# Optimization experiments

Hardware: AMD Instinct MI355X
Metric: run time of the kernel (lower is better)

Reference implementation:

```python
import jax, jax.numpy as jnp
import numpy as np

N = 50000
E = 800000


def gcn_layer(x, W, b, row, col):
    # Linear transform first (as in CustomGCNLayer.forward)
    h = x @ W + b  # [N, out]
    # Segment-mean over incoming edges grouped by destination node `col`;
    # out[i] = mean(h[row[col == i]]) if node i has in-edges else h[i].
    s = jax.ops.segment_sum(h[row], col, num_segments=N)              # [N, out]
    cnt = jax.ops.segment_sum(jnp.ones((row.shape[0],), h.dtype), col, num_segments=N)  # [N]
    mean = s / jnp.maximum(cnt, 1.0)[:, None]
    return jnp.where(cnt[:, None] > 0, mean, h)


def setup_inputs() -> dict:
    key = jax.random.key(0)
    ks = jax.random.split(key, 6)
    x = jax.random.normal(ks[0], (N, 128), dtype=jnp.float32)
    edge_index = jax.random.randint(ks[1], (2, E), 0, N, dtype=jnp.int64)
    # Glorot-ish scaled weights
    W1 = jax.random.normal(ks[2], (128, 128), dtype=jnp.float32) * (1.0 / np.sqrt(128))
    b1 = jnp.zeros((128,), jnp.float32)
    W2 = jax.random.normal(ks[3], (128, 128), dtype=jnp.float32) * (1.0 / np.sqrt(128))
    b2 = jnp.zeros((128,), jnp.float32)
    W3 = jax.random.normal(ks[4], (128, 64), dtype=jnp.float32) * (1.0 / np.sqrt(128))
    b3 = jnp.zeros((64,), jnp.float32)
    return {"x": x, "edge_index": edge_index, "W1": W1, "b1": b1,
            "W2": W2, "b2": b2, "W3": W3, "b3": b3}


def reference(x, edge_index, W1, b1, W2, b2, W3, b3):
    row, col = edge_index[0], edge_index[1]
    h = jax.nn.relu(gcn_layer(x, W1, b1, row, col))
    # Dropout layers run in eval mode for the reference (identity).
    h = jax.nn.relu(gcn_layer(h, W2, b2, row, col))
    h = gcn_layer(h, W3, b3, row, col)
    return jax.nn.log_softmax(h, axis=1)
```

## Files before the change

### kernel.cpp

```cpp
#include <hip/hip_runtime.h>
#include <hip/hip_bf16.h>


typedef __attribute__((ext_vector_type(8))) short short8v;
typedef __attribute__((ext_vector_type(4))) float f32x4;

#define NPART 256

static __device__ __forceinline__ ushort f2bf(float f) {
    __hip_bfloat16 h = __float2bfloat16(f);
    return *reinterpret_cast<ushort*>(&h);
}
static __device__ __forceinline__ float bf_lo(uint u) { return __uint_as_float(u << 16); }
static __device__ __forceinline__ float bf_hi(uint u) { return __uint_as_float(u & 0xffff0000u); }

static __device__ __forceinline__ void gemm1_body(
    const float* __restrict__ X, const float* __restrict__ W,
    const float* __restrict__ bias, ushort* __restrict__ Y, int n,
    int wid, int lane) {
    int r0 = wid * 16;
    if (r0 >= n) return;
    int arow = r0 + (lane & 15);
    if (arow >= n) arow = n - 1;
    int kb = lane >> 4;
    int c  = lane & 15;

    f32x4 acc[8];
#pragma unroll
    for (int ct = 0; ct < 8; ++ct) acc[ct] = (f32x4)(0.f);

#pragma unroll
    for (int kt = 0; kt < 4; ++kt) {
        const float* ap = &X[(size_t)arow * 128 + kt * 32 + kb * 8];
        float4 a0 = *(const float4*)ap;
        float4 a1 = *(const float4*)(ap + 4);
        union { short8v v; ushort u[8]; } av;
        av.u[0] = f2bf(a0.x); av.u[1] = f2bf(a0.y);
        av.u[2] = f2bf(a0.z); av.u[3] = f2bf(a0.w);
        av.u[4] = f2bf(a1.x); av.u[5] = f2bf(a1.y);
        av.u[6] = f2bf(a1.z); av.u[7] = f2bf(a1.w);
#pragma unroll
        for (int ct = 0; ct < 8; ++ct) {
            union { short8v v; ushort u[8]; } bv;
#pragma unroll
            for (int j = 0; j < 8; ++j)
                bv.u[j] = f2bf(W[(size_t)(kt * 32 + kb * 8 + j) * 128 + ct * 16 + c]);
            acc[ct] = __builtin_amdgcn_mfma_f32_16x16x32_bf16(av.v, bv.v, acc[ct], 0, 0, 0);
        }
    }

    int rg = lane >> 4;
#pragma unroll
    for (int ct = 0; ct < 8; ++ct) {
        float bvs = bias[ct * 16 + c];
#pragma unroll
        for (int j = 0; j < 4; ++j) {
            int r = r0 + rg * 4 + j;
            if (r < n) Y[(size_t)r * 128 + ct * 16 + c] = f2bf(acc[ct][j] + bvs);
        }
    }
}

__global__ __launch_bounds__(256) void fused_pa(
    const int* __restrict__ col, int* __restrict__ Gmat,
    const float* __restrict__ x, const float* __restrict__ W1,
    const float* __restrict__ b1, ushort* __restrict__ hbuf,
    const float* __restrict__ W2, ushort* __restrict__ Wf2,
    const float* __restrict__ W3, ushort* __restrict__ Wf3,
    int n, int E, int NBKT, int ECH, int GB) {
    __shared__ uint hist[1024];
    int b = blockIdx.x, t = threadIdx.x;
    if (b < NPART) {
        for (int i = t; i < NBKT; i += 256) hist[i] = 0;
        __syncthreads();
        int e0 = b * ECH, e1 = min(e0 + ECH, E);
        for (int e = e0 + t; e < e1; e += 256)
            atomicAdd(&hist[col[e] >> 6], 1u);
        __syncthreads();
        for (int i = t; i < NBKT; i += 256)
            Gmat[i * NPART + b] = (int)hist[i];
        return;
    }
    b -= NPART;
    if (b < GB) {
        int wid = (b * 256 + t) >> 6;
        gemm1_body(x, W1, b1, hbuf, n, wid, t & 63);
        return;
    }
    b -= GB;
    const float* W; ushort* Wf; int OUT; int tid;
    if (b < 8) { W = W2; Wf = Wf2; OUT = 128; tid = b * 256 + t; }
    else       { W = W3; Wf = Wf3; OUT = 64;  tid = (b - 8) * 256 + t; }
    int CT = OUT >> 4;
    int total = 4 * CT * 64;
    if (tid >= total) return;
    int kt   = tid / (CT * 64);
    int rem  = tid % (CT * 64);
    int ct   = rem >> 6;
    int lane = rem & 63;
    int c  = lane & 15;
    int kb = lane >> 4;
    ushort tmp[8];
#pragma unroll
    for (int j = 0; j < 8; ++j)
        tmp[j] = f2bf(W[(kt * 32 + kb * 8 + j) * OUT + ct * 16 + c]);
    uint4 o;
    o.x = ((uint)tmp[1] << 16) | tmp[0];
    o.y = ((uint)tmp[3] << 16) | tmp[2];
    o.z = ((uint)tmp[5] << 16) | tmp[4];
    o.w = ((uint)tmp[7] << 16) | tmp[6];
    ((uint4*)Wf)[tid] = o;
}

__global__ void scanA_partial(const int* __restrict__ g, int* __restrict__ bsum, int M) {
    __shared__ int lds[256];
    int i = blockIdx.x * 256 + threadIdx.x;
    int v = (i < M) ? g[i] : 0;
    lds[threadIdx.x] = v;
    __syncthreads();
    for (int s = 128; s > 0; s >>= 1) {
        if (threadIdx.x < s) lds[threadIdx.x] += lds[threadIdx.x + s];
        __syncthreads();
    }
    if (threadIdx.x == 0) bsum[blockIdx.x] = lds[0];
}

__global__ void scan_bsums_big(int* __restrict__ bsum, int nb) {
    __shared__ int ts[256];
    int t = threadIdx.x;
    int v[4]; int s = 0;
#pragma unroll
    for (int j = 0; j < 4; ++j) {
        int i = t * 4 + j;
        v[j] = (i < nb) ? bsum[i] : 0;
        s += v[j];
    }
    ts[t] = s;
    __syncthreads();
    for (int off = 1; off < 256; off <<= 1) {
        int u = (t >= off) ? ts[t - off] : 0;
        __syncthreads();
        ts[t] += u;
        __syncthreads();
    }
    int run = ts[t] - s;
#pragma unroll
    for (int j = 0; j < 4; ++j) {
        int i = t * 4 + j;
        if (i < nb) { int old = v[j]; bsum[i] = run; run += old; }
    }
}

__global__ void scanA_final(int* __restrict__ g, const int* __restrict__ bsum, int M) {
    __shared__ int lds[256];
    int t = threadIdx.x;
    int i = blockIdx.x * 256 + t;
    int v = (i < M) ? g[i] : 0;
    lds[t] = v;
    __syncthreads();
    for (int off = 1; off < 256; off <<= 1) {
        int u = (t >= off) ? lds[t - off] : 0;
        __syncthreads();
        lds[t] += u;
        __syncthreads();
    }
    if (i < M) g[i] = lds[t] - v + bsum[blockIdx.x];
}

__global__ __launch_bounds__(256) void pa2_scatter(
    const int* __restrict__ row, const int* __restrict__ col,
    const int* __restrict__ Gscan, uint* __restrict__ coarse,
    int E, int NBKT, int ECH) {
    __shared__ uint cur[1024];
    int p = blockIdx.x, t = threadIdx.x;
    for (int i = t; i < NBKT; i += 256) cur[i] = (uint)Gscan[i * NPART + p];
    __syncthreads();
    int e0 = p * ECH, e1 = min(e0 + ECH, E);
    for (int e = e0 + t; e < e1; e += 256) {
        int d = col[e];
        uint slot = atomicAdd(&cur[d >> 6], 1u);
        coarse[slot] = ((uint)(d & 63) << 16) | (uint)(row[e] & 0xFFFF);
    }
}

__global__ __launch_bounds__(256) void pb_fine(
    const uint* __restrict__ coarse, const int* __restrict__ Gscan,
    int* __restrict__ cnt, int* __restrict__ start,
    ushort* __restrict__ srclist16, int n, int E, int NBKT) {
    __shared__ uint c64[64];
    int b = blockIdx.x, t = threadIdx.x;
    int lo = Gscan[b * NPART];
    int hi = (b + 1 < NBKT) ? Gscan[(b + 1) * NPART] : E;
    if (t < 64) c64[t] = 0;
    __syncthreads();
    for (int i = lo + t; i < hi; i += 256)
        atomicAdd(&c64[coarse[i] >> 16], 1u);
    __syncthreads();
    if (t < 64) {
        uint v = c64[t];
        uint x = v;
#pragma unroll
        for (int off = 1; off < 64; off <<= 1) {
            uint u = __shfl_up(x, off);
            if (t >= off) x += u;
        }
        uint excl = x - v;
        int node = b * 64 + t;
        if (node < n) { cnt[node] = (int)v; start[node] = lo + (int)excl; }
        c64[t] = excl;
    }
    __syncthreads();
    for (int i = lo + t; i < hi; i += 256) {
        uint u  = coarse[i];
        uint dl = u >> 16;
        uint slot = atomicAdd(&c64[dl], 1u);
        srclist16[lo + slot] = (ushort)u;
    }
}

template <int OUT>
__global__ __launch_bounds__(256) void gemm_mfma(
    const ushort* __restrict__ X, const ushort* __restrict__ Wf,
    const float* __restrict__ bias, ushort* __restrict__ Y, int n) {
    constexpr int CT = OUT / 16;
    int wid  = (blockIdx.x * 256 + threadIdx.x) >> 6;
    int lane = threadIdx.x & 63;
    int r0 = wid * 16;
    if (r0 >= n) return;
    int arow = r0 + (lane & 15);
    if (arow >= n) arow = n - 1;
    int kb = lane >> 4;

    f32x4 acc[CT];
#pragma unroll
    for (int ct = 0; ct < CT; ++ct) acc[ct] = (f32x4)(0.f);

#pragma unroll
    for (int kt = 0; kt < 4; ++kt) {
        short8v a = *(const short8v*)&X[(size_t)arow * 128 + kt * 32 + kb * 8];
#pragma unroll
        for (int ct = 0; ct < CT; ++ct) {
            short8v b = *(const short8v*)&Wf[(size_t)((kt * CT + ct) * 64 + lane) * 8];
            acc[ct] = __builtin_amdgcn_mfma_f32_16x16x32_bf16(a, b, acc[ct], 0, 0, 0);
        }
    }

    int c  = lane & 15;
    int rg = lane >> 4;
#pragma unroll
    for (int ct = 0; ct < CT; ++ct) {
        float bv = bias[ct * 16 + c];
#pragma unroll
        for (int j = 0; j < 4; ++j) {
            int r = r0 + rg * 4 + j;
            if (r < n) Y[(size_t)r * OUT + ct * 16 + c] = f2bf(acc[ct][j] + bv);
        }
    }
}

template <bool RELU>
__global__ __launch_bounds__(256) void agg128_bf16(
    const ushort* __restrict__ h, const int* __restrict__ start,
    const int* __restrict__ cnt, const ushort* __restrict__ srclist16,
    ushort* __restrict__ out, int n) {
    int wid  = (blockIdx.x * blockDim.x + threadIdx.x) >> 6;
    int lane = threadIdx.x & 63;
    if (wid >= n) return;
    const uint* h32 = (const uint*)h;
    int s0 = start[wid];
    int c  = cnt[wid];
    float ax = 0.f, ay = 0.f;
    for (int base = 0; base < c; base += 64) {
        int m = c - base;
        if (m > 64) m = 64;
        int idx = (int)srclist16[s0 + base + (lane < m ? lane : 0)];
        int e = 0;
        for (; e + 8 <= m; e += 8) {
            int i0 = __shfl(idx, e + 0), i1 = __shfl(idx, e + 1);
            int i2 = __shfl(idx, e + 2), i3 = __shfl(idx, e + 3);
            int i4 = __shfl(idx, e + 4), i5 = __shfl(idx, e + 5);
            int i6 = __shfl(idx, e + 6), i7 = __shfl(idx, e + 7);
            uint u0 = h32[(size_t)i0 * 64 + lane];
            uint u1 = h32[(size_t)i1 * 64 + lane];
            uint u2 = h32[(size_t)i2 * 64 + lane];
            uint u3 = h32[(size_t)i3 * 64 + lane];
            uint u4 = h32[(size_t)i4 * 64 + lane];
            uint u5 = h32[(size_t)i5 * 64 + lane];
            uint u6 = h32[(size_t)i6 * 64 + lane];
            uint u7 = h32[(size_t)i7 * 64 + lane];
            ax += ((bf_lo(u0) + bf_lo(u1)) + (bf_lo(u2) + bf_lo(u3))) +
                  ((bf_lo(u4) + bf_lo(u5)) + (bf_lo(u6) + bf_lo(u7)));
            ay += ((bf_hi(u0) + bf_hi(u1)) + (bf_hi(u2) + bf_hi(u3))) +
                  ((bf_hi(u4) + bf_hi(u5)) + (bf_hi(u6) + bf_hi(u7)));
        }
        for (; e + 4 <= m; e += 4) {
            int i0 = __shfl(idx, e + 0), i1 = __shfl(idx, e + 1);
            int i2 = __shfl(idx, e + 2), i3 = __shfl(idx, e + 3);
            uint u0 = h32[(size_t)i0 * 64 + lane];
            uint u1 = h32[(size_t)i1 * 64 + lane];
            uint u2 = h32[(size_t)i2 * 64 + lane];
            uint u3 = h32[(size_t)i3 * 64 + lane];
            ax += (bf_lo(u0) + bf_lo(u1)) + (bf_lo(u2) + bf_lo(u3));
            ay += (bf_hi(u0) + bf_hi(u1)) + (bf_hi(u2) + bf_hi(u3));
        }
        for (; e < m; ++e) {
            int i0 = __shfl(idx, e);
            uint u0 = h32[(size_t)i0 * 64 + lane];
            ax += bf_lo(u0);
            ay += bf_hi(u0);
        }
    }
    float rx, ry;
    if (c > 0) {
        float inv = 1.f / (float)c;
        rx = ax * inv; ry = ay * inv;
    } else {
        uint u = h32[(size_t)wid * 64 + lane];
        rx = bf_lo(u); ry = bf_hi(u);
    }
    if (RELU) { rx = fmaxf(rx, 0.f); ry = fmaxf(ry, 0.f); }
    ((uint*)out)[(size_t)wid * 64 + lane] = ((uint)f2bf(ry) << 16) | f2bf(rx);
}

__global__ __launch_bounds__(256) void agg64_lsm_bf16(
    const ushort* __restrict__ h, const int* __restrict__ start,
    const int* __restrict__ cnt, const ushort* __restrict__ srclist16,
    float* __restrict__ out, int n) {
    int wid  = (blockIdx.x * blockDim.x + threadIdx.x) >> 6;
    int lane = threadIdx.x & 63;
    if (wid >= n) return;
    int s0 = start[wid];
    int c  = cnt[wid];
    float a = 0.f;
    for (int base = 0; base < c; base += 64) {
        int m = c - base;
        if (m > 64) m = 64;
        int idx = (int)srclist16[s0 + base + (lane < m ? lane : 0)];
        int e = 0;
        for (; e + 8 <= m; e += 8) {
            int i0 = __shfl(idx, e + 0), i1 = __shfl(idx, e + 1);
            int i2 = __shfl(idx, e + 2), i3 = __shfl(idx, e + 3);
            int i4 = __shfl(idx, e + 4), i5 = __shfl(idx, e + 5);
            int i6 = __shfl(idx, e + 6), i7 = __shfl(idx, e + 7);
            float v0 = __uint_as_float((uint)h[(size_t)i0 * 64 + lane] << 16);
            float v1 = __uint_as_float((uint)h[(size_t)i1 * 64 + lane] << 16);
            float v2 = __uint_as_float((uint)h[(size_t)i2 * 64 + lane] << 16);
            float v3 = __uint_as_float((uint)h[(size_t)i3 * 64 + lane] << 16);
            float v4 = __uint_as_float((uint)h[(size_t)i4 * 64 + lane] << 16);
            float v5 = __uint_as_float((uint)h[(size_t)i5 * 64 + lane] << 16);
            float v6 = __uint_as_float((uint)h[(size_t)i6 * 64 + lane] << 16);
            float v7 = __uint_as_float((uint)h[(size_t)i7 * 64 + lane] << 16);
            a += ((v0 + v1) + (v2 + v3)) + ((v4 + v5) + (v6 + v7));
        }
        for (; e < m; ++e) {
            int i0 = __shfl(idx, e);
            a += __uint_as_float((uint)h[(size_t)i0 * 64 + lane] << 16);
        }
    }
    float v = (c > 0) ? a / (float)c
                      : __uint_as_float((uint)h[(size_t)wid * 64 + lane] << 16);

    float m = v;
#pragma unroll
    for (int off = 32; off > 0; off >>= 1) m = fmaxf(m, __shfl_xor(m, off));
    float ex = __expf(v - m);
    float s = ex;
#pragma unroll
    for (int off = 32; off > 0; off >>= 1) s += __shfl_xor(s, off);
    out[(size_t)wid * 64 + lane] = v - m - __logf(s);
}

extern "C" void kernel_launch(void* const* d_in, const int* in_sizes, int n_in,
                              void* d_out, int out_size, void* d_ws, size_t ws_size,
                              hipStream_t stream) {
    const float* x  = (const float*)d_in[0];
    const int*   ei = (const int*)d_in[1];
    const float* W1 = (const float*)d_in[2];
    const float* b1 = (const float*)d_in[3];
    const float* W2 = (const float*)d_in[4];
    const float* b2 = (const float*)d_in[5];
    const float* W3 = (const float*)d_in[6];
    const float* b3 = (const float*)d_in[7];
    float* out = (float*)d_out;

    const int n = in_sizes[0] / 128;
    const int E = in_sizes[1] / 2;
    const int* row = ei;
    const int* col = ei + E;

    char* ws = (char*)d_ws;
    size_t off = 0;
    auto carve = [&](size_t bytes) {
        char* p = ws + off;
        off = (off + bytes + 255) & ~(size_t)255;
        return p;
    };
    ushort* hbuf      = (ushort*)carve((size_t)n * 128 * 2);
    ushort* abuf      = (ushort*)carve((size_t)n * 128 * 2);
    ushort* Wf2       = (ushort*)carve(4 * 8 * 64 * 8 * 2);
    ushort* Wf3       = (ushort*)carve(4 * 4 * 64 * 8 * 2);
    const int NBKT    = (n + 63) / 64;
    int*    Gmat      = (int*)carve((size_t)NBKT * NPART * sizeof(int));
    uint*   coarse    = (uint*)carve((size_t)E * sizeof(uint));
    int*    cnt       = (int*)carve((size_t)n * sizeof(int));
    int*    start     = (int*)carve((size_t)n * sizeof(int));
    ushort* srclist16 = (ushort*)carve((size_t)E * 2);
    int*    bsum      = (int*)carve(4096);

    const int ECH   = (E + NPART - 1) / NPART;
    const int M     = NBKT * NPART;
    const int MB    = (M + 255) / 256;
    const int nwave = (n + 15) / 16;
    const int GB    = (nwave + 3) / 4;
    const int agrid = (n + 3) / 4;

    fused_pa<<<NPART + GB + 12, 256, 0, stream>>>(col, Gmat, x, W1, b1, hbuf,
                                                  W2, Wf2, W3, Wf3,
                                                  n, E, NBKT, ECH, GB);
    scanA_partial<<<MB, 256, 0, stream>>>(Gmat, bsum, M);
    scan_bsums_big<<<1, 256, 0, stream>>>(bsum, MB);
    scanA_final<<<MB, 256, 0, stream>>>(Gmat, bsum, M);
    pa2_scatter<<<NPART, 256, 0, stream>>>(row, col, Gmat, coarse, E, NBKT, ECH);
    pb_fine<<<NBKT, 256, 0, stream>>>(coarse, Gmat, cnt, start, srclist16, n, E, NBKT);

    agg128_bf16<true><<<agrid, 256, 0, stream>>>(hbuf, start, cnt, srclist16, abuf, n);
    gemm_mfma<128><<<GB, 256, 0, stream>>>(abuf, Wf2, b2, hbuf, n);
    agg128_bf16<true><<<agrid, 256, 0, stream>>>(hbuf, start, cnt, srclist16, abuf, n);
    gemm_mfma<64><<<GB, 256, 0, stream>>>(abuf, Wf3, b3, hbuf, n);
    agg64_lsm_bf16<<<agrid, 256, 0, stream>>>(hbuf, start, cnt, srclist16, out, n);
}
```

Baseline: 168.3 us.

## Fuse neighbor aggregation with following MFMA GEMM via shared-memory tile

Replaces the separate agg128 and gemm_mfma kernels for layers 2 and 3 with one kernel. Each block aggregates 16 nodes (4 per wave) into an LDS tile, then the four waves split the output columns for the MFMA GEMM. This removes the round-trip of the aggregated bf16 activations through global memory and two kernel launches. In exchange, the sequential per-node aggregation now sits in front of a block-wide barrier, which can lower latency hiding. Each 16-row tile is also spread across waves, so fewer columns are computed per wave.

```diff
diff --git a/kernel.cpp b/kernel.cpp
--- a/kernel.cpp
+++ b/kernel.cpp
@@ -218,58 +218,10 @@
     }
 }
 
-template <int OUT>
-__global__ __launch_bounds__(256) void gemm_mfma(
-    const ushort* __restrict__ X, const ushort* __restrict__ Wf,
-    const float* __restrict__ bias, ushort* __restrict__ Y, int n) {
-    constexpr int CT = OUT / 16;
-    int wid  = (blockIdx.x * 256 + threadIdx.x) >> 6;
-    int lane = threadIdx.x & 63;
-    int r0 = wid * 16;
-    if (r0 >= n) return;
-    int arow = r0 + (lane & 15);
-    if (arow >= n) arow = n - 1;
-    int kb = lane >> 4;
-
-    f32x4 acc[CT];
-#pragma unroll
-    for (int ct = 0; ct < CT; ++ct) acc[ct] = (f32x4)(0.f);
-
-#pragma unroll
-    for (int kt = 0; kt < 4; ++kt) {
-        short8v a = *(const short8v*)&X[(size_t)arow * 128 + kt * 32 + kb * 8];
-#pragma unroll
-        for (int ct = 0; ct < CT; ++ct) {
-            short8v b = *(const short8v*)&Wf[(size_t)((kt * CT + ct) * 64 + lane) * 8];
-            acc[ct] = __builtin_amdgcn_mfma_f32_16x16x32_bf16(a, b, acc[ct], 0, 0, 0);
-        }
-    }
-
-    int c  = lane & 15;
-    int rg = lane >> 4;
-#pragma unroll
-    for (int ct = 0; ct < CT; ++ct) {
-        float bv = bias[ct * 16 + c];
-#pragma unroll
-        for (int j = 0; j < 4; ++j) {
-            int r = r0 + rg * 4 + j;
-            if (r < n) Y[(size_t)r * OUT + ct * 16 + c] = f2bf(acc[ct][j] + bv);
-        }
-    }
-}
-
-template <bool RELU>
-__global__ __launch_bounds__(256) void agg128_bf16(
-    const ushort* __restrict__ h, const int* __restrict__ start,
-    const int* __restrict__ cnt, const ushort* __restrict__ srclist16,
-    ushort* __restrict__ out, int n) {
-    int wid  = (blockIdx.x * blockDim.x + threadIdx.x) >> 6;
-    int lane = threadIdx.x & 63;
-    if (wid >= n) return;
-    const uint* h32 = (const uint*)h;
-    int s0 = start[wid];
-    int c  = cnt[wid];
-    float ax = 0.f, ay = 0.f;
+static __device__ __forceinline__ void agg_node128(
+    const uint* __restrict__ h32, const ushort* __restrict__ srclist16,
+    int s0, int c, int lane, float& ax, float& ay) {
+    ax = 0.f; ay = 0.f;
     for (int base = 0; base < c; base += 64) {
         int m = c - base;
         if (m > 64) m = 64;
@@ -310,16 +262,76 @@
             ay += bf_hi(u0);
         }
     }
-    float rx, ry;
-    if (c > 0) {
-        float inv = 1.f / (float)c;
-        rx = ax * inv; ry = ay * inv;
-    } else {
-        uint u = h32[(size_t)wid * 64 + lane];
-        rx = bf_lo(u); ry = bf_hi(u);
-    }
-    if (RELU) { rx = fmaxf(rx, 0.f); ry = fmaxf(ry, 0.f); }
-    ((uint*)out)[(size_t)wid * 64 + lane] = ((uint)f2bf(ry) << 16) | f2bf(rx);
+}
+
+template <int OUT>
+__global__ __launch_bounds__(256) void fused_agg_gemm(
+    const ushort* __restrict__ h, const int* __restrict__ start,
+    const int* __restrict__ cnt, const ushort* __restrict__ srclist16,
+    const ushort* __restrict__ Wf, const float* __restrict__ bias,
+    ushort* __restrict__ Y, int n) {
+    constexpr int CT  = OUT / 16;
+    constexpr int CTW = CT / 4;
+    __shared__ uint tile[16 * 68];
+    int t = threadIdx.x;
+    int wave = t >> 6, lane = t & 63;
+    int base = blockIdx.x * 16;
+    if (base >= n) return;
+    const uint* h32 = (const uint*)h;
+
+#pragma unroll
+    for (int q = 0; q < 4; ++q) {
+        int r = wave * 4 + q;
+        int node = base + r;
+        uint pk = 0;
+        if (node < n) {
+            int s0 = start[node], c = cnt[node];
+            float ax, ay;
+            agg_node128(h32, srclist16, s0, c, lane, ax, ay);
+            float rx, ry;
+            if (c > 0) {
+                float inv = 1.f / (float)c;
+                rx = ax * inv; ry = ay * inv;
+            } else {
+                uint u = h32[(size_t)node * 64 + lane];
+                rx = bf_lo(u); ry = bf_hi(u);
+            }
+            rx = fmaxf(rx, 0.f); ry = fmaxf(ry, 0.f);
+            pk = ((uint)f2bf(ry) << 16) | f2bf(rx);
+        }
+        tile[r * 68 + lane] = pk;
+    }
+    __syncthreads();
+
+    int ar = lane & 15;
+    int kb = lane >> 4;
+    f32x4 acc[CTW];
+#pragma unroll
+    for (int j = 0; j < CTW; ++j) acc[j] = (f32x4)(0.f);
+
+#pragma unroll
+    for (int kt = 0; kt < 4; ++kt) {
+        uint4 a4 = *(const uint4*)&tile[ar * 68 + kt * 16 + kb * 4];
+        short8v a = *(const short8v*)&a4;
+#pragma unroll
+        for (int j = 0; j < CTW; ++j) {
+            int ct = wave * CTW + j;
+            short8v b = *(const short8v*)&Wf[(size_t)((kt * CT + ct) * 64 + lane) * 8];
+            acc[j] = __builtin_amdgcn_mfma_f32_16x16x32_bf16(a, b, acc[j], 0, 0, 0);
+        }
+    }
+
+    int c16 = lane & 15, rg = lane >> 4;
+#pragma unroll
+    for (int j = 0; j < CTW; ++j) {
+        int ct = wave * CTW + j;
+        float bv = bias[ct * 16 + c16];
+#pragma unroll
+        for (int jj = 0; jj < 4; ++jj) {
+            int r = base + rg * 4 + jj;
+            if (r < n) Y[(size_t)r * OUT + ct * 16 + c16] = f2bf(acc[j][jj] + bv);
+        }
+    }
 }
 
 __global__ __launch_bounds__(256) void agg64_lsm_bf16(
@@ -412,6 +424,7 @@
     const int MB    = (M + 255) / 256;
     const int nwave = (n + 15) / 16;
     const int GB    = (nwave + 3) / 4;
+    const int FB    = (n + 15) / 16;
     const int agrid = (n + 3) / 4;
 
     fused_pa<<<NPART + GB + 12, 256, 0, stream>>>(col, Gmat, x, W1, b1, hbuf,
@@ -423,9 +436,9 @@
     pa2_scatter<<<NPART, 256, 0, stream>>>(row, col, Gmat, coarse, E, NBKT, ECH);
     pb_fine<<<NBKT, 256, 0, stream>>>(coarse, Gmat, cnt, start, srclist16, n, E, NBKT);
 
-    agg128_bf16<true><<<agrid, 256, 0, stream>>>(hbuf, start, cnt, srclist16, abuf, n);
-    gemm_mfma<128><<<GB, 256, 0, stream>>>(abuf, Wf2, b2, hbuf, n);
-    agg128_bf16<true><<<agrid, 256, 0, stream>>>(hbuf, start, cnt, srclist16, abuf, n);
-    gemm_mfma<64><<<GB, 256, 0, stream>>>(abuf, Wf3, b3, hbuf, n);
+    fused_agg_gemm<128><<<FB, 256, 0, stream>>>(hbuf, start, cnt, srclist16,
+                                                Wf2, b2, abuf, n);
+    fused_agg_gemm<64><<<FB, 256, 0, stream>>>(abuf, start, cnt, srclist16,
+                                               Wf3, b3, hbuf, n);
     agg64_lsm_bf16<<<agrid, 256, 0, stream>>>(hbuf, start, cnt, srclist16, out, n);
 }
```

After: 149.9 us. 10.9% less time.

## Slice feature columns across XCDs in aggregation to improve L2 locality

Applied to the files above, without the earlier changes.

Replaces the one-wave-per-node 128-wide aggregation with a grid-stride kernel of 2048 blocks. Each block is pinned to one quarter of the feature columns, chosen from blockIdx bits so that blocks landing on the same XCD gather only that slice of h. Each wave splits its 64 lanes into 4 edge groups of 16 column lanes and reduces them with cross-lane shuffles. The goal is to shrink each XCD's gather working set so it fits in that XCD's L2 and to reduce random HBM traffic. The cost is that every edge index is reread four times and there are extra shuffle reductions, with only 16 lanes doing the final store.

```diff
diff --git a/kernel.cpp b/kernel.cpp
--- a/kernel.cpp
+++ b/kernel.cpp
@@ -218,6 +218,65 @@
     }
 }
 
+__global__ __launch_bounds__(256) void agg_sliced(
+    const ushort* __restrict__ h, const int* __restrict__ start,
+    const int* __restrict__ cnt, const ushort* __restrict__ srclist16,
+    ushort* __restrict__ out, int n) {
+    int b = blockIdx.x, t = threadIdx.x;
+    int wave = t >> 6, lane = t & 63;
+    int s    = (b & 7) >> 1;
+    int wis  = ((b >> 3) * 2 + (b & 1)) * 4 + wave;
+    int stride = gridDim.x;
+    const uint* h32 = (const uint*)h;
+    uint* out32 = (uint*)out;
+    int g     = lane >> 4;
+    int sbase = s * 16 + (lane & 15);
+
+    for (int d = wis; d < n; d += stride) {
+        int s0 = start[d], c = cnt[d];
+        float ax = 0.f, ay = 0.f;
+        for (int base = 0; base < c; base += 64) {
+            int m = c - base; if (m > 64) m = 64;
+            int idx = (int)srclist16[s0 + base + (lane < m ? lane : 0)];
+            int e = 0;
+            for (; e + 16 <= m; e += 16) {
+                int i0 = __shfl(idx, e + g);
+                int i1 = __shfl(idx, e + 4 + g);
+                int i2 = __shfl(idx, e + 8 + g);
+                int i3 = __shfl(idx, e + 12 + g);
+                uint u0 = h32[(size_t)i0 * 64 + sbase];
+                uint u1 = h32[(size_t)i1 * 64 + sbase];
+                uint u2 = h32[(size_t)i2 * 64 + sbase];
+                uint u3 = h32[(size_t)i3 * 64 + sbase];
+                ax += (bf_lo(u0) + bf_lo(u1)) + (bf_lo(u2) + bf_lo(u3));
+                ay += (bf_hi(u0) + bf_hi(u1)) + (bf_hi(u2) + bf_hi(u3));
+            }
+            for (; e + 8 <= m; e += 8) {
+                int i0 = __shfl(idx, e + g);
+                int i1 = __shfl(idx, e + 4 + g);
+                uint u0 = h32[(size_t)i0 * 64 + sbase];
+                uint u1 = h32[(size_t)i1 * 64 + sbase];
+                ax += bf_lo(u0) + bf_lo(u1);
+                ay += bf_hi(u0) + bf_hi(u1);
+            }
+            for (; e < m; e += 4) {
+                int i0 = __shfl(idx, e + g);
+                uint u0 = (e + g < m) ? h32[(size_t)i0 * 64 + sbase] : 0u;
+                ax += bf_lo(u0);
+                ay += bf_hi(u0);
+            }
+        }
+        ax += __shfl_xor(ax, 16); ay += __shfl_xor(ay, 16);
+        ax += __shfl_xor(ax, 32); ay += __shfl_xor(ay, 32);
+        float rx, ry;
+        if (c > 0) { float inv = 1.f / (float)c; rx = ax * inv; ry = ay * inv; }
+        else { uint u = h32[(size_t)d * 64 + sbase]; rx = bf_lo(u); ry = bf_hi(u); }
+        rx = fmaxf(rx, 0.f); ry = fmaxf(ry, 0.f);
+        if (lane < 16)
+            out32[(size_t)d * 64 + sbase] = ((uint)f2bf(ry) << 16) | f2bf(rx);
+    }
+}
+
 template <int OUT>
 __global__ __launch_bounds__(256) void gemm_mfma(
     const ushort* __restrict__ X, const ushort* __restrict__ Wf,
@@ -256,70 +315,6 @@
             if (r < n) Y[(size_t)r * OUT + ct * 16 + c] = f2bf(acc[ct][j] + bv);
         }
     }
-}
-
-template <bool RELU>
-__global__ __launch_bounds__(256) void agg128_bf16(
-    const ushort* __restrict__ h, const int* __restrict__ start,
-    const int* __restrict__ cnt, const ushort* __restrict__ srclist16,
-    ushort* __restrict__ out, int n) {
-    int wid  = (blockIdx.x * blockDim.x + threadIdx.x) >> 6;
-    int lane = threadIdx.x & 63;
-    if (wid >= n) return;
-    const uint* h32 = (const uint*)h;
-    int s0 = start[wid];
-    int c  = cnt[wid];
-    float ax = 0.f, ay = 0.f;
-    for (int base = 0; base < c; base += 64) {
-        int m = c - base;
-        if (m > 64) m = 64;
-        int idx = (int)srclist16[s0 + base + (lane < m ? lane : 0)];
-        int e = 0;
-        for (; e + 8 <= m; e += 8) {
-            int i0 = __shfl(idx, e + 0), i1 = __shfl(idx, e + 1);
-            int i2 = __shfl(idx, e + 2), i3 = __shfl(idx, e + 3);
-            int i4 = __shfl(idx, e + 4), i5 = __shfl(idx, e + 5);
-            int i6 = __shfl(idx, e + 6), i7 = __shfl(idx, e + 7);
-            uint u0 = h32[(size_t)i0 * 64 + lane];
-            uint u1 = h32[(size_t)i1 * 64 + lane];
-            uint u2 = h32[(size_t)i2 * 64 + lane];
-            uint u3 = h32[(size_t)i3 * 64 + lane];
-            uint u4 = h32[(size_t)i4 * 64 + lane];
-            uint u5 = h32[(size_t)i5 * 64 + lane];
-            uint u6 = h32[(size_t)i6 * 64 + lane];
-            uint u7 = h32[(size_t)i7 * 64 + lane];
-            ax += ((bf_lo(u0) + bf_lo(u1)) + (bf_lo(u2) + bf_lo(u3))) +
-                  ((bf_lo(u4) + bf_lo(u5)) + (bf_lo(u6) + bf_lo(u7)));
-            ay += ((bf_hi(u0) + bf_hi(u1)) + (bf_hi(u2) + bf_hi(u3))) +
-                  ((bf_hi(u4) + bf_hi(u5)) + (bf_hi(u6) + bf_hi(u7)));
-        }
-        for (; e + 4 <= m; e += 4) {
-            int i0 = __shfl(idx, e + 0), i1 = __shfl(idx, e + 1);
-            int i2 = __shfl(idx, e + 2), i3 = __shfl(idx, e + 3);
-            uint u0 = h32[(size_t)i0 * 64 + lane];
-            uint u1 = h32[(size_t)i1 * 64 + lane];
-            uint u2 = h32[(size_t)i2 * 64 + lane];
-            uint u3 = h32[(size_t)i3 * 64 + lane];
-            ax += (bf_lo(u0) + bf_lo(u1)) + (bf_lo(u2) + bf_lo(u3));
-            ay += (bf_hi(u0) + bf_hi(u1)) + (bf_hi(u2) + bf_hi(u3));
-        }
-        for (; e < m; ++e) {
-            int i0 = __shfl(idx, e);
-            uint u0 = h32[(size_t)i0 * 64 + lane];
-            ax += bf_lo(u0);
-            ay += bf_hi(u0);
-        }
-    }
-    float rx, ry;
-    if (c > 0) {
-        float inv = 1.f / (float)c;
-        rx = ax * inv; ry = ay * inv;
-    } else {
-        uint u = h32[(size_t)wid * 64 + lane];
-        rx = bf_lo(u); ry = bf_hi(u);
-    }
-    if (RELU) { rx = fmaxf(rx, 0.f); ry = fmaxf(ry, 0.f); }
-    ((uint*)out)[(size_t)wid * 64 + lane] = ((uint)f2bf(ry) << 16) | f2bf(rx);
 }
 
 __global__ __launch_bounds__(256) void agg64_lsm_bf16(
@@ -423,9 +418,9 @@
     pa2_scatter<<<NPART, 256, 0, stream>>>(row, col, Gmat, coarse, E, NBKT, ECH);
     pb_fine<<<NBKT, 256, 0, stream>>>(coarse, Gmat, cnt, start, srclist16, n, E, NBKT);
 
-    agg128_bf16<true><<<agrid, 256, 0, stream>>>(hbuf, start, cnt, srclist16, abuf, n);
+    agg_sliced<<<2048, 256, 0, stream>>>(hbuf, start, cnt, srclist16, abuf, n);
     gemm_mfma<128><<<GB, 256, 0, stream>>>(abuf, Wf2, b2, hbuf, n);
-    agg128_bf16<true><<<agrid, 256, 0, stream>>>(hbuf, start, cnt, srclist16, abuf, n);
+    agg_sliced<<<2048, 256, 0, stream>>>(hbuf, start, cnt, srclist16, abuf, n);
     gemm_mfma<64><<<GB, 256, 0, stream>>>(abuf, Wf3, b3, hbuf, n);
     agg64_lsm_bf16<<<agrid, 256, 0, stream>>>(hbuf, start, cnt, srclist16, out, n);
 }
```

Measured after the change: 221.6 us. 31.7% more time.
